# Optimization experiments

Measured on AMD Instinct MI355X. Metric: run time of the kernel, lower is better.

## Reference

```python
import jax, jax.numpy as jnp
import numpy as np
from jax import lax

B, H, W, DIM = 64, 32, 32, 448
HEADS, DH, WS = 8, 28, 8
INNER = DH * HEADS            # 224
C2 = DIM // 2                 # 224 (spatial branch channels == inner_dim)
HALF = INNER // 2             # 112 per attention sub-branch
SEQ_L1 = WS * WS              # 64 tokens per window
SEQ_L2 = (256 // HEADS) ** 2 // SEQ_L1  # 16 == number of windows (32x32 map)
SCALE = DH ** -0.5


def setup_inputs() -> dict:
    key = jax.random.key(0)
    ks = jax.random.split(key, 18)
    def nrm(k, shape, s):
        return jax.random.normal(k, shape, jnp.float32) * s
    inp = {}
    inp["x"] = jax.random.normal(ks[0], (B, H, W, DIM), jnp.float32)
    # trunc_normal_(std=1) positional biases -> clipped normals
    inp["pos_emb1"] = jnp.clip(jax.random.normal(ks[1], (1, 1, HEADS // 2, SEQ_L1, SEQ_L1), jnp.float32), -2.0, 2.0)
    inp["pos_emb2"] = jnp.clip(jax.random.normal(ks[2], (1, 1, HEADS // 2, SEQ_L2, SEQ_L2), jnp.float32), -2.0, 2.0)
    # linear weights stored (in, out)
    inp["Wq"] = nrm(ks[3], (C2, INNER), 0.02)
    inp["Wkv"] = nrm(ks[4], (C2, 2 * INNER), 0.02)
    inp["Wout"] = nrm(ks[5], (INNER, DIM), 0.02)
    inp["bout"] = nrm(ks[6], (DIM,), 0.02)
    # 3D conv weights (O, I, D, Kh, Kw), fan-in = 224*27 -> std ~ 0.01
    for i, name in enumerate(["convr", "conv1", "conv2", "conv3"]):
        inp[name + "_w"] = nrm(ks[7 + 2 * i], (C2, C2, 3, 3, 3), 0.01)
        inp[name + "_b"] = nrm(ks[8 + 2 * i], (C2,), 0.01)
    return inp


def _conv3d(t, w, b):
    y = lax.conv_general_dilated(t, w, (1, 1, 1), [(1, 1)] * 3,
                                 dimension_numbers=("NCDHW", "OIDHW", "NCDHW"))
    return y + b[None, :, None, None, None]


def _window(t):
    # [b, H, W, c] -> [b, n_windows, ws*ws, c]
    b, h, w, c = t.shape
    t = t.reshape(b, h // WS, WS, w // WS, WS, c).transpose(0, 1, 3, 2, 4, 5)
    return t.reshape(b, (h // WS) * (w // WS), WS * WS, c)


def _unwindow(t):
    # [b, n_windows, ws*ws, c] -> [b, H, W, c]
    b, n, m, c = t.shape
    t = t.reshape(b, H // WS, W // WS, WS, WS, c).transpose(0, 1, 3, 2, 4, 5)
    return t.reshape(b, H, W, c)


def _split_heads(t):
    # [b, n, m, half] -> [b, n, heads//2, m, dh]
    b, n, m, c = t.shape
    return t.reshape(b, n, m, HEADS // 2, DH).transpose(0, 1, 3, 2, 4)


def _merge_heads(t):
    # [b, n, heads//2, m, dh] -> [b, n, m, half]
    b, n, h, m, d = t.shape
    return t.transpose(0, 1, 3, 2, 4).reshape(b, n, m, h * d)


def _attn(q, q_, k, v, pos):
    del q_
    sim = jnp.einsum("bnhid,bnhjd->bnhij", q * SCALE, k) + pos
    a = jax.nn.softmax(sim, axis=-1)
    return jnp.einsum("bnhij,bnhjd->bnhid", a, v)


def reference(x, pos_emb1, pos_emb2, Wq, Wkv, Wout, bout,
              convr_w, convr_b, conv1_w, conv1_b, conv2_w, conv2_b, conv3_w, conv3_b):
    b = x.shape[0]
    x1 = x[..., :C2]
    x2 = x[..., C2:]
    # spectral 3D conv branch: [b, c2, 1, H, W]
    x2 = x2.transpose(0, 3, 1, 2)[:, :, None]
    res = jax.nn.relu(_conv3d(x2, convr_w, convr_b))
    o = jax.nn.relu(_conv3d(x2, conv1_w, conv1_b))
    o = jax.nn.relu(_conv3d(o, conv2_w, conv2_b))
    o = jax.nn.relu(_conv3d(o, conv3_w, conv3_b))
    X2S = (o + res)[:, :, 0].transpose(0, 2, 3, 1)  # [b, H, W, c2]

    q = x1 @ Wq
    kv = x1 @ Wkv
    k, v = kv[..., :INNER], kv[..., INNER:]
    q1, q2 = q[..., :HALF], q[..., HALF:]
    k1, k2 = k[..., :HALF], k[..., HALF:]
    v1, v2 = v[..., :HALF], v[..., HALF:]

    # local (within-window) branch
    q1h, k1h, v1h = map(lambda t: _split_heads(_window(t)), (q1, k1, v1))
    sim1 = jnp.einsum("bnhid,bnhjd->bnhij", q1h * SCALE, k1h) + pos_emb1
    out1 = jnp.einsum("bnhij,bnhjd->bnhid", jax.nn.softmax(sim1, axis=-1), v1h)
    out1 = _merge_heads(out1)  # [b, n, m, half]

    # grid (across-window) branch: swap window/token axes
    q2h, k2h, v2h = map(lambda t: _split_heads(_window(t).transpose(0, 2, 1, 3)), (q2, k2, v2))
    sim2 = jnp.einsum("bnhid,bnhjd->bnhij", q2h * SCALE, k2h) + pos_emb2
    out2 = jnp.einsum("bnhij,bnhjd->bnhid", jax.nn.softmax(sim2, axis=-1), v2h)
    out2 = _merge_heads(out2).transpose(0, 2, 1, 3)  # [b, n, m, half]

    out = jnp.concatenate([out1, out2], axis=-1) @ Wout + bout  # [b, n, m, DIM]
    out = _unwindow(out)
    return jnp.concatenate([out, X2S], axis=-1)  # [b, H, W, DIM + C2]
```

## Files before the change

### kernel.cpp

```cpp
#include <hip/hip_runtime.h>

typedef unsigned short u16;
typedef unsigned int   u32;
typedef __attribute__((ext_vector_type(4))) float  f32x4;
typedef __attribute__((ext_vector_type(8))) short  s16x8;
typedef __attribute__((ext_vector_type(8))) __bf16 bf16x8;
typedef __attribute__((ext_vector_type(2))) u32    u32x2;

#define DEV __device__ __forceinline__
#define SCALE_Q 0.1889822365046136f

DEV float bf2f(u16 u){ u32 x = ((u32)u)<<16; float f; __builtin_memcpy(&f,&x,4); return f; }
DEV u16   f2bf(float f){ u32 x; __builtin_memcpy(&x,&f,4); return (u16)((x + 0x7fffu + ((x>>16)&1u))>>16); }

DEV s16x8 cvt8(const float* __restrict__ src){
  f32x4 f0 = *(const f32x4*)src, f1 = *(const f32x4*)(src+4);
  bf16x8 b;
  b[0]=(__bf16)f0[0]; b[1]=(__bf16)f0[1]; b[2]=(__bf16)f0[2]; b[3]=(__bf16)f0[3];
  b[4]=(__bf16)f1[0]; b[5]=(__bf16)f1[1]; b[6]=(__bf16)f1[2]; b[7]=(__bf16)f1[3];
  return __builtin_bit_cast(s16x8, b);
}

DEV void ld28(const u16* __restrict__ p, float* dst, float scale){
#pragma unroll
  for (int j=0;j<7;j++){
    u32x2 w = *(const u32x2*)(p + j*4);
    dst[j*4+0] = bf2f((u16)(w[0]&0xffffu))*scale;
    dst[j*4+1] = bf2f((u16)(w[0]>>16))*scale;
    dst[j*4+2] = bf2f((u16)(w[1]&0xffffu))*scale;
    dst[j*4+3] = bf2f((u16)(w[1]>>16))*scale;
  }
}

__global__ void pack_k(const float* __restrict__ Wq, const float* __restrict__ Wkv,
                       const float* __restrict__ Wout,
                       const float* __restrict__ wr, const float* __restrict__ w1,
                       const float* __restrict__ w2, const float* __restrict__ w3,
                       u16* __restrict__ WqkvT, u16* __restrict__ WoutT,
                       u16* __restrict__ convW)
{
  int idx = blockIdx.x*256 + threadIdx.x;
  if (idx < 150528) {
    int nn = idx/224, k = idx - nn*224;
    float v;
    if (nn < 224)      v = Wq [k*224 + nn];
    else if (nn < 448) v = Wkv[k*448 + (nn-224)];
    else               v = Wkv[k*448 + (nn-448) + 224];
    WqkvT[idx] = f2bf(v);
  } else if (idx < 250880) {
    int j = idx - 150528;
    int nn = j/224, k = j - nn*224;
    WoutT[j] = f2bf(Wout[k*448 + nn]);
  } else {
    int j = idx - 250880;
    int cv = j/451584, rem = j - cv*451584;
    int co = rem/2016, kk = rem - co*2016;
    int tap = kk/224, ci = kk - tap*224;
    const float* w = (cv==0)?wr:(cv==1)?w1:(cv==2)?w2:w3;
    convW[j] = f2bf(w[(co*224 + ci)*27 + 9 + tap]);
  }
}

enum { M_QKV=0, M_CX2=1, M_CBF=2, M_C3=3, M_OUT=4 };

template<int MODE>
__global__ __launch_bounds__(512,2) void gemm_k(
    const void* __restrict__ Av, const u16* __restrict__ Bt,
    const float* __restrict__ bias, const u16* __restrict__ resid,
    void* __restrict__ Dv)
{
  constexpr bool CONV = (MODE==M_CX2 || MODE==M_CBF || MODE==M_C3);
  constexpr bool AF32 = (MODE==M_QKV || MODE==M_CX2);
  constexpr int KTOT = CONV ? 2016 : 224;
  constexpr int KS   = KTOT/32;
  constexpr int ASTR = AF32 ? 448 : 224;
  constexpr int AOFF = (MODE==M_CX2) ? 224 : 0;

  __shared__ __align__(16) u16 Als[128][40];
  __shared__ __align__(16) u16 Bls[224][40];

  const int t  = threadIdx.x;
  const int bm = blockIdx.x, nb = blockIdx.y;
  const int lane = t&63, lr = lane&15, lg = lane>>4;
  const int w = t>>6, wm = w>>1, wn = w&1;
  const int ar = t>>2, aq = t&3;
  const int p  = bm*128 + ar;
  const int pb = p>>10, py = (p>>5)&31, px = p&31;

  f32x4 acc[2][7];
  { f32x4 zf = {0.f,0.f,0.f,0.f};
#pragma unroll
    for (int i=0;i<2;i++)
#pragma unroll
      for (int j=0;j<7;j++) acc[i][j] = zf; }

  const s16x8 zv = {0,0,0,0,0,0,0,0};

  for (int ks=0; ks<KS; ++ks) {
    s16x8 av;
    if constexpr (CONV) {
      const int tap = ks/7, kc = ks - tap*7;
      const int dy = tap/3 - 1, dx = tap - (tap/3)*3 - 1;
      const int yy = py+dy, xx = px+dx;
      const bool ok = (yy>=0) & (yy<32) & (xx>=0) & (xx<32);
      const int yyc = yy<0?0:(yy>31?31:yy);
      const int xxc = xx<0?0:(xx>31?31:xx);
      const int off = ((pb*32+yyc)*32+xxc)*ASTR + AOFF + kc*32 + aq*8;
      s16x8 val;
      if constexpr (AF32) val = cvt8((const float*)Av + off);
      else                val = *(const s16x8*)((const u16*)Av + off);
      av = ok ? val : zv;
    } else {
      const int off = p*ASTR + ks*32 + aq*8;
      if constexpr (AF32) av = cvt8((const float*)Av + off);
      else                av = *(const s16x8*)((const u16*)Av + off);
    }
    const s16x8 bv0 = *(const s16x8*)(Bt + (nb*224 + (t>>2))*KTOT + ks*32 + aq*8);
    s16x8 bv1 = zv;
    if (t < 384)
      bv1 = *(const s16x8*)(Bt + (nb*224 + 128 + (t>>2))*KTOT + ks*32 + aq*8);

    __syncthreads();
    *(s16x8*)&Als[ar][aq*8] = av;
    *(s16x8*)&Bls[t>>2][aq*8] = bv0;
    if (t < 384) *(s16x8*)&Bls[128 + (t>>2)][aq*8] = bv1;
    __syncthreads();

    const bf16x8 af0 = *(const bf16x8*)&Als[wm*32 +      lr][lg*8];
    const bf16x8 af1 = *(const bf16x8*)&Als[wm*32 + 16 + lr][lg*8];
#pragma unroll
    for (int ni=0; ni<7; ++ni) {
      const bf16x8 bfr = *(const bf16x8*)&Bls[wn*112 + ni*16 + lr][lg*8];
      acc[0][ni] = __builtin_amdgcn_mfma_f32_16x16x32_bf16(af0, bfr, acc[0][ni], 0,0,0);
      acc[1][ni] = __builtin_amdgcn_mfma_f32_16x16x32_bf16(af1, bfr, acc[1][ni], 0,0,0);
    }
  }

#pragma unroll
  for (int mi=0; mi<2; ++mi) {
    const int rbase = bm*128 + wm*32 + mi*16 + lg*4;
#pragma unroll
    for (int ni=0; ni<7; ++ni) {
      const int col = wn*112 + ni*16 + lr;
      const int n   = nb*224 + col;
      float badd = 0.f;
      if constexpr (MODE != M_QKV) badd = bias[n];
#pragma unroll
      for (int r=0;r<4;r++){
        const int prow = rbase + r;
        float v = acc[mi][ni][r] + badd;
        if constexpr (CONV) v = fmaxf(v, 0.f);
        if constexpr (MODE==M_C3) {
          v += bf2f(resid[prow*224 + col]);
          ((float*)Dv)[prow*672 + 448 + col] = v;
        } else if constexpr (MODE==M_OUT) {
          ((float*)Dv)[prow*672 + n] = v;
        } else if constexpr (MODE==M_QKV) {
          ((u16*)Dv)[prow*672 + n] = f2bf(v);
        } else {
          ((u16*)Dv)[prow*224 + col] = f2bf(v);
        }
      }
    }
  }
}

__global__ __launch_bounds__(256,2) void attn1_k(const u16* __restrict__ qkv,
    const float* __restrict__ pos1, u16* __restrict__ attnout)
{
  __shared__ __align__(16) float KL[64][112];
  __shared__ __align__(16) float VL[64][112];
  const int t = threadIdx.x;
  const int b = blockIdx.x>>4, n = blockIdx.x&15;
  const int base = b*1024 + (n>>2)*256 + (n&3)*8;
  {
    const int r = t>>2, part = t&3;
    const int pr_ = base + (r>>3)*32 + (r&7);
    const u16* kp = qkv + pr_*672 + 224 + part*28;
    const u16* vp = kp + 224;
#pragma unroll
    for (int j=0;j<7;j++){
      u32x2 kk = *(const u32x2*)(kp + j*4);
      u32x2 vv = *(const u32x2*)(vp + j*4);
      const int c = part*28 + j*4;
      KL[r][c+0]=bf2f((u16)(kk[0]&0xffffu)); KL[r][c+1]=bf2f((u16)(kk[0]>>16));
      KL[r][c+2]=bf2f((u16)(kk[1]&0xffffu)); KL[r][c+3]=bf2f((u16)(kk[1]>>16));
      VL[r][c+0]=bf2f((u16)(vv[0]&0xffffu)); VL[r][c+1]=bf2f((u16)(vv[0]>>16));
      VL[r][c+2]=bf2f((u16)(vv[1]&0xffffu)); VL[r][c+3]=bf2f((u16)(vv[1]>>16));
    }
  }
  __syncthreads();

  const int h = t>>6, i = t&63;
  const int pi = base + (i>>3)*32 + (i&7);
  float q[28];
  ld28(qkv + pi*672 + h*28, q, SCALE_Q);

  float s[64];
  const float* pr = pos1 + (h*64+i)*64;
#pragma unroll
  for (int j4=0;j4<16;j4++){
    f32x4 pv = *(const f32x4*)(pr + j4*4);
    s[j4*4+0]=pv[0]; s[j4*4+1]=pv[1]; s[j4*4+2]=pv[2]; s[j4*4+3]=pv[3];
  }
  const int c0 = h*28;
#pragma unroll
  for (int j=0;j<64;j++){
    const f32x4* kr = (const f32x4*)&KL[j][c0];
    float a0=0.f,a1=0.f,a2=0.f,a3=0.f;
#pragma unroll
    for (int u=0;u<7;u++){
      f32x4 kv = kr[u];
      a0 += q[u*4+0]*kv[0]; a1 += q[u*4+1]*kv[1];
      a2 += q[u*4+2]*kv[2]; a3 += q[u*4+3]*kv[3];
    }
    s[j] += (a0+a1)+(a2+a3);
  }
  float mx = s[0];
#pragma unroll
  for (int j=1;j<64;j++) mx = fmaxf(mx, s[j]);
  float sum = 0.f;
#pragma unroll
  for (int j=0;j<64;j++){ float e = __expf(s[j]-mx); s[j]=e; sum+=e; }
  const float inv = 1.f/sum;

  float out[28];
#pragma unroll
  for (int u=0;u<28;u++) out[u]=0.f;
#pragma unroll
  for (int j=0;j<64;j++){
    const float pj = s[j];
    const f32x4* vr = (const f32x4*)&VL[j][c0];
#pragma unroll
    for (int u=0;u<7;u++){
      f32x4 vv = vr[u];
      out[u*4+0] += pj*vv[0]; out[u*4+1] += pj*vv[1];
      out[u*4+2] += pj*vv[2]; out[u*4+3] += pj*vv[3];
    }
  }
  u16* op = attnout + pi*224 + h*28;
#pragma unroll
  for (int u=0;u<7;u++){
    u32x2 wv;
    wv[0] = (u32)f2bf(out[u*4+0]*inv) | ((u32)f2bf(out[u*4+1]*inv)<<16);
    wv[1] = (u32)f2bf(out[u*4+2]*inv) | ((u32)f2bf(out[u*4+3]*inv)<<16);
    *(u32x2*)(op + u*4) = wv;
  }
}

__global__ __launch_bounds__(256,1) void attn2_k(const u16* __restrict__ qkv,
    const float* __restrict__ pos2, u16* __restrict__ attnout)
{
  const int t = threadIdx.x;
  const int b = blockIdx.x>>4, mg = blockIdx.x&15;
  const int m = mg*4 + (t>>6);
  const int lane = t&63, h = lane>>4, i = lane&15;
  const int base = b*1024 + (m>>3)*32 + (m&7);
  const int pi = base + (i>>2)*256 + (i&3)*8;

  float q[28];
  ld28(qkv + pi*672 + 112 + h*28, q, SCALE_Q);

  float s[16];
  const float* pr = pos2 + (h*16+i)*16;
#pragma unroll
  for (int j4=0;j4<4;j4++){
    f32x4 pv = *(const f32x4*)(pr + j4*4);
    s[j4*4+0]=pv[0]; s[j4*4+1]=pv[1]; s[j4*4+2]=pv[2]; s[j4*4+3]=pv[3];
  }
#pragma unroll
  for (int j=0;j<16;j++){
    const int pj_ = base + (j>>2)*256 + (j&3)*8;
    float kk[28];
    ld28(qkv + pj_*672 + 336 + h*28, kk, 1.0f);
    float a=0.f;
#pragma unroll
    for (int u=0;u<28;u++) a += q[u]*kk[u];
    s[j] += a;
  }
  float mx = s[0];
#pragma unroll
  for (int j=1;j<16;j++) mx = fmaxf(mx, s[j]);
  float sum = 0.f;
#pragma unroll
  for (int j=0;j<16;j++){ float e = __expf(s[j]-mx); s[j]=e; sum+=e; }
  const float inv = 1.f/sum;

  float out[28];
#pragma unroll
  for (int u=0;u<28;u++) out[u]=0.f;
#pragma unroll
  for (int j=0;j<16;j++){
    const int pj_ = base + (j>>2)*256 + (j&3)*8;
    float vv[28];
    ld28(qkv + pj_*672 + 560 + h*28, vv, 1.0f);
    const float pj = s[j];
#pragma unroll
    for (int u=0;u<28;u++) out[u] += pj*vv[u];
  }
  u16* op = attnout + pi*224 + 112 + h*28;
#pragma unroll
  for (int u=0;u<7;u++){
    u32x2 wv;
    wv[0] = (u32)f2bf(out[u*4+0]*inv) | ((u32)f2bf(out[u*4+1]*inv)<<16);
    wv[1] = (u32)f2bf(out[u*4+2]*inv) | ((u32)f2bf(out[u*4+3]*inv)<<16);
    *(u32x2*)(op + u*4) = wv;
  }
}

extern "C" void kernel_launch(void* const* d_in, const int* in_sizes, int n_in,
                              void* d_out, int out_size, void* d_ws, size_t ws_size,
                              hipStream_t stream) {
  const float* x    = (const float*)d_in[0];
  const float* pos1 = (const float*)d_in[1];
  const float* pos2 = (const float*)d_in[2];
  const float* Wq   = (const float*)d_in[3];
  const float* Wkv  = (const float*)d_in[4];
  const float* Wout = (const float*)d_in[5];
  const float* bout = (const float*)d_in[6];
  const float* wr   = (const float*)d_in[7];
  const float* br   = (const float*)d_in[8];
  const float* w1   = (const float*)d_in[9];
  const float* b1   = (const float*)d_in[10];
  const float* w2   = (const float*)d_in[11];
  const float* b2   = (const float*)d_in[12];
  const float* w3   = (const float*)d_in[13];
  const float* b3   = (const float*)d_in[14];

  char* ws = (char*)d_ws;
  const size_t SLOT = 65536ull*224*2;
  u16* res  = (u16*)(ws);
  u16* oA   = (u16*)(ws + SLOT);
  u16* oB   = (u16*)(ws + 2*SLOT);
  u16* qkv  = (u16*)(ws);
  u16* attnout = (u16*)(ws + 3*SLOT);
  u16* WqkvT   = (u16*)(ws + 4*SLOT);
  u16* WoutT   = WqkvT + 672*224;
  u16* convW   = WoutT + 448*224;
  float* dout  = (float*)d_out;

  pack_k<<<8036, 256, 0, stream>>>(Wq, Wkv, Wout, wr, w1, w2, w3, WqkvT, WoutT, convW);

  gemm_k<M_CX2><<<dim3(512,1), 512, 0, stream>>>(x,  convW + 0*451584, br, nullptr, res);
  gemm_k<M_CX2><<<dim3(512,1), 512, 0, stream>>>(x,  convW + 1*451584, b1, nullptr, oA);
  gemm_k<M_CBF><<<dim3(512,1), 512, 0, stream>>>(oA, convW + 2*451584, b2, nullptr, oB);
  gemm_k<M_C3 ><<<dim3(512,1), 512, 0, stream>>>(oB, convW + 3*451584, b3, res, dout);

  gemm_k<M_QKV><<<dim3(512,3), 512, 0, stream>>>(x, WqkvT, nullptr, nullptr, qkv);
  attn1_k<<<1024, 256, 0, stream>>>(qkv, pos1, attnout);
  attn2_k<<<1024, 256, 0, stream>>>(qkv, pos2, attnout);
  gemm_k<M_OUT><<<dim3(512,2), 512, 0, stream>>>(attnout, WoutT, bout, nullptr, dout);
}
```

Measured before the change: 555.1 us.

## Pad conv inputs, fuse first two convs, double-buffer GEMM with direct-to-LDS loads

```diff
diff --git a/kernel.cpp b/kernel.cpp
--- a/kernel.cpp
+++ b/kernel.cpp
@@ -19,6 +19,13 @@
   b[0]=(__bf16)f0[0]; b[1]=(__bf16)f0[1]; b[2]=(__bf16)f0[2]; b[3]=(__bf16)f0[3];
   b[4]=(__bf16)f1[0]; b[5]=(__bf16)f1[1]; b[6]=(__bf16)f1[2]; b[7]=(__bf16)f1[3];
   return __builtin_bit_cast(s16x8, b);
+}
+
+DEV void gll16(const u16* g, u16* l){
+  __builtin_amdgcn_global_load_lds(
+      (const __attribute__((address_space(1))) u32*)(const void*)g,
+      (__attribute__((address_space(3))) u32*)(void*)l,
+      16, 0, 0);
 }
 
 DEV void ld28(const u16* __restrict__ p, float* dst, float scale){
@@ -61,104 +68,143 @@
   }
 }
 
-enum { M_QKV=0, M_CX2=1, M_CBF=2, M_C3=3, M_OUT=4 };
+__global__ void prep_k(const float* __restrict__ x, u16* __restrict__ x1bf,
+                       u16* __restrict__ xpad, u16* __restrict__ oApad,
+                       u16* __restrict__ oBpad)
+{
+  int idx = blockIdx.x*256 + threadIdx.x;
+  int pp = idx/28, c8 = idx - pp*28;
+  int b = pp/1156, rem = pp - b*1156, y = rem/34, xx = rem - y*34;
+  int c0 = c8*8;
+  if (y>=1 && y<=32 && xx>=1 && xx<=32){
+    int p = (b*32 + y-1)*32 + (xx-1);
+    *(s16x8*)(x1bf + p*224 + c0) = cvt8(x + p*448 + c0);
+    *(s16x8*)(xpad + pp*224 + c0) = cvt8(x + p*448 + 224 + c0);
+  } else {
+    const s16x8 z = {0,0,0,0,0,0,0,0};
+    *(s16x8*)(xpad  + pp*224 + c0) = z;
+    *(s16x8*)(oApad + pp*224 + c0) = z;
+    *(s16x8*)(oBpad + pp*224 + c0) = z;
+  }
+}
+
+enum { M_FUSED=0, M_C2=1, M_C3=2, M_QKV=3, M_OUT=4 };
 
 template<int MODE>
-__global__ __launch_bounds__(512,2) void gemm_k(
-    const void* __restrict__ Av, const u16* __restrict__ Bt,
-    const float* __restrict__ bias, const u16* __restrict__ resid,
-    void* __restrict__ Dv)
+__global__ __launch_bounds__(512,1) void gemm_k(
+    const u16* __restrict__ A, const u16* __restrict__ Bt,
+    const float* __restrict__ bias0, const float* __restrict__ bias1,
+    u16* __restrict__ outA, u16* __restrict__ outB, float* __restrict__ outF)
 {
-  constexpr bool CONV = (MODE==M_CX2 || MODE==M_CBF || MODE==M_C3);
-  constexpr bool AF32 = (MODE==M_QKV || MODE==M_CX2);
+  constexpr bool CONV = (MODE==M_FUSED || MODE==M_C2 || MODE==M_C3);
   constexpr int KTOT = CONV ? 2016 : 224;
   constexpr int KS   = KTOT/32;
-  constexpr int ASTR = AF32 ? 448 : 224;
-  constexpr int AOFF = (MODE==M_CX2) ? 224 : 0;
-
-  __shared__ __align__(16) u16 Als[128][40];
-  __shared__ __align__(16) u16 Bls[224][40];
+
+  __shared__ __align__(16) u16 Als[2][256*32];
+  __shared__ __align__(16) u16 Bls[2][224*32];
 
   const int t  = threadIdx.x;
   const int bm = blockIdx.x, nb = blockIdx.y;
   const int lane = t&63, lr = lane&15, lg = lane>>4;
   const int w = t>>6, wm = w>>1, wn = w&1;
-  const int ar = t>>2, aq = t&3;
-  const int p  = bm*128 + ar;
-  const int pb = p>>10, py = (p>>5)&31, px = p&31;
-
-  f32x4 acc[2][7];
+  const int aq8 = (t&3)*8;
+
+  const int r0 = t>>2;
+  const int p0 = bm*256 + r0, p1 = p0 + 128;
+  int PP0=0, PP1=0;
+  if constexpr (CONV){
+    PP0 = ((p0>>10)*34 + ((p0>>5)&31) + 1)*34 + (p0&31) + 1;
+    PP1 = ((p1>>10)*34 + ((p1>>5)&31) + 1)*34 + (p1&31) + 1;
+  }
+  const int Bb0 = (nb*224 +       r0)*KTOT + aq8;
+  const int Bb1 = (nb*224 + 128 + r0)*KTOT + aq8;
+
+  u16* aL[2] = { &Als[0][0] + w*512, &Als[1][0] + w*512 };
+  u16* bL[2] = { &Bls[0][0] + w*512, &Bls[1][0] + w*512 };
+
+  auto STAGE = [&](int buf, int ks){
+    if constexpr (CONV){
+      const int tap = ks/7, kc = ks - tap*7;
+      const int ty = tap/3, tx = tap - ty*3;
+      const int toff = (ty-1)*34 + (tx-1);
+      const int ke = kc*32 + aq8;
+      gll16(A + (PP0+toff)*224 + ke, aL[buf]);
+      gll16(A + (PP1+toff)*224 + ke, aL[buf] + 4096);
+    } else {
+      gll16(A + p0*224 + ks*32 + aq8, aL[buf]);
+      gll16(A + p1*224 + ks*32 + aq8, aL[buf] + 4096);
+    }
+    gll16(Bt + Bb0 + ks*32, bL[buf]);
+    if (w < 6) gll16(Bt + Bb1 + ks*32, bL[buf] + 4096);
+  };
+
+  f32x4 acc[4][7];
   { f32x4 zf = {0.f,0.f,0.f,0.f};
 #pragma unroll
-    for (int i=0;i<2;i++)
+    for (int i=0;i<4;i++)
 #pragma unroll
       for (int j=0;j<7;j++) acc[i][j] = zf; }
 
-  const s16x8 zv = {0,0,0,0,0,0,0,0};
-
-  for (int ks=0; ks<KS; ++ks) {
-    s16x8 av;
-    if constexpr (CONV) {
-      const int tap = ks/7, kc = ks - tap*7;
-      const int dy = tap/3 - 1, dx = tap - (tap/3)*3 - 1;
-      const int yy = py+dy, xx = px+dx;
-      const bool ok = (yy>=0) & (yy<32) & (xx>=0) & (xx<32);
-      const int yyc = yy<0?0:(yy>31?31:yy);
-      const int xxc = xx<0?0:(xx>31?31:xx);
-      const int off = ((pb*32+yyc)*32+xxc)*ASTR + AOFF + kc*32 + aq*8;
-      s16x8 val;
-      if constexpr (AF32) val = cvt8((const float*)Av + off);
-      else                val = *(const s16x8*)((const u16*)Av + off);
-      av = ok ? val : zv;
-    } else {
-      const int off = p*ASTR + ks*32 + aq*8;
-      if constexpr (AF32) av = cvt8((const float*)Av + off);
-      else                av = *(const s16x8*)((const u16*)Av + off);
-    }
-    const s16x8 bv0 = *(const s16x8*)(Bt + (nb*224 + (t>>2))*KTOT + ks*32 + aq*8);
-    s16x8 bv1 = zv;
-    if (t < 384)
-      bv1 = *(const s16x8*)(Bt + (nb*224 + 128 + (t>>2))*KTOT + ks*32 + aq*8);
+  STAGE(0, 0);
+  __syncthreads();
+
+  for (int ks=0; ks<KS; ++ks){
+    const int cur = ks&1;
+    if (ks+1 < KS) STAGE(cur^1, ks+1);
+
+    const u16* Ac = &Als[cur][0];
+    const u16* Bc = &Bls[cur][0];
+    bf16x8 af[4], bfv[7];
+#pragma unroll
+    for (int mi=0; mi<4; ++mi)
+      af[mi] = *(const bf16x8*)(Ac + (wm*64 + mi*16 + lr)*32 + lg*8);
+#pragma unroll
+    for (int ni=0; ni<7; ++ni)
+      bfv[ni] = *(const bf16x8*)(Bc + (wn*112 + ni*16 + lr)*32 + lg*8);
+
+#pragma unroll
+    for (int ni=0; ni<7; ++ni)
+#pragma unroll
+      for (int mi=0; mi<4; ++mi)
+        acc[mi][ni] = __builtin_amdgcn_mfma_f32_16x16x32_bf16(af[mi], bfv[ni], acc[mi][ni], 0,0,0);
 
     __syncthreads();
-    *(s16x8*)&Als[ar][aq*8] = av;
-    *(s16x8*)&Bls[t>>2][aq*8] = bv0;
-    if (t < 384) *(s16x8*)&Bls[128 + (t>>2)][aq*8] = bv1;
-    __syncthreads();
-
-    const bf16x8 af0 = *(const bf16x8*)&Als[wm*32 +      lr][lg*8];
-    const bf16x8 af1 = *(const bf16x8*)&Als[wm*32 + 16 + lr][lg*8];
-#pragma unroll
-    for (int ni=0; ni<7; ++ni) {
-      const bf16x8 bfr = *(const bf16x8*)&Bls[wn*112 + ni*16 + lr][lg*8];
-      acc[0][ni] = __builtin_amdgcn_mfma_f32_16x16x32_bf16(af0, bfr, acc[0][ni], 0,0,0);
-      acc[1][ni] = __builtin_amdgcn_mfma_f32_16x16x32_bf16(af1, bfr, acc[1][ni], 0,0,0);
-    }
-  }
-
-#pragma unroll
-  for (int mi=0; mi<2; ++mi) {
-    const int rbase = bm*128 + wm*32 + mi*16 + lg*4;
-#pragma unroll
-    for (int ni=0; ni<7; ++ni) {
+  }
+
+  const float* bs;
+  if constexpr (MODE==M_FUSED) bs = (nb==0) ? bias0 : bias1;
+  else bs = bias0;
+
+#pragma unroll
+  for (int mi=0; mi<4; ++mi){
+    const int rbase = bm*256 + wm*64 + mi*16 + lg*4;
+#pragma unroll
+    for (int ni=0; ni<7; ++ni){
       const int col = wn*112 + ni*16 + lr;
-      const int n   = nb*224 + col;
-      float badd = 0.f;
-      if constexpr (MODE != M_QKV) badd = bias[n];
 #pragma unroll
       for (int r=0;r<4;r++){
-        const int prow = rbase + r;
-        float v = acc[mi][ni][r] + badd;
-        if constexpr (CONV) v = fmaxf(v, 0.f);
-        if constexpr (MODE==M_C3) {
-          v += bf2f(resid[prow*224 + col]);
-          ((float*)Dv)[prow*672 + 448 + col] = v;
-        } else if constexpr (MODE==M_OUT) {
-          ((float*)Dv)[prow*672 + n] = v;
-        } else if constexpr (MODE==M_QKV) {
-          ((u16*)Dv)[prow*672 + n] = f2bf(v);
+        const int row = rbase + r;
+        float v = acc[mi][ni][r];
+        if constexpr (MODE==M_FUSED){
+          v = fmaxf(v + bs[col], 0.f);
+          if (nb==0){
+            outF[row*672 + 448 + col] = v;
+          } else {
+            const int pp = ((row>>10)*34 + ((row>>5)&31) + 1)*34 + (row&31) + 1;
+            outB[pp*224 + col] = f2bf(v);
+          }
+        } else if constexpr (MODE==M_C2){
+          v = fmaxf(v + bs[col], 0.f);
+          const int pp = ((row>>10)*34 + ((row>>5)&31) + 1)*34 + (row&31) + 1;
+          outB[pp*224 + col] = f2bf(v);
+        } else if constexpr (MODE==M_C3){
+          v = fmaxf(v + bs[col], 0.f);
+          const int o = row*672 + 448 + col;
+          outF[o] = v + outF[o];
+        } else if constexpr (MODE==M_QKV){
+          outA[row*672 + nb*224 + col] = f2bf(v);
         } else {
-          ((u16*)Dv)[prow*224 + col] = f2bf(v);
+          outF[row*672 + nb*224 + col] = v + bs[nb*224 + col];
         }
       }
     }
@@ -328,26 +374,28 @@
   const float* b3   = (const float*)d_in[14];
 
   char* ws = (char*)d_ws;
-  const size_t SLOT = 65536ull*224*2;
-  u16* res  = (u16*)(ws);
-  u16* oA   = (u16*)(ws + SLOT);
-  u16* oB   = (u16*)(ws + 2*SLOT);
-  u16* qkv  = (u16*)(ws);
-  u16* attnout = (u16*)(ws + 3*SLOT);
-  u16* WqkvT   = (u16*)(ws + 4*SLOT);
-  u16* WoutT   = WqkvT + 672*224;
-  u16* convW   = WoutT + 448*224;
+  const size_t PADSZ = 73984ull*224*2;
+  const size_t FLATS = 65536ull*224*2;
+  u16* xpad   = (u16*)(ws);
+  u16* oApad  = (u16*)(ws + PADSZ);
+  u16* oBpad  = (u16*)(ws + 2*PADSZ);
+  u16* x1bf   = (u16*)(ws + 3*PADSZ);
+  u16* convW  = (u16*)(ws + 3*PADSZ + FLATS);
+  u16* WqkvT  = convW + 4*451584;
+  u16* WoutT  = WqkvT + 672*224;
+  u16* qkv     = (u16*)(ws);
+  u16* attnout = (u16*)(ws + 88080384);
   float* dout  = (float*)d_out;
 
   pack_k<<<8036, 256, 0, stream>>>(Wq, Wkv, Wout, wr, w1, w2, w3, WqkvT, WoutT, convW);
-
-  gemm_k<M_CX2><<<dim3(512,1), 512, 0, stream>>>(x,  convW + 0*451584, br, nullptr, res);
-  gemm_k<M_CX2><<<dim3(512,1), 512, 0, stream>>>(x,  convW + 1*451584, b1, nullptr, oA);
-  gemm_k<M_CBF><<<dim3(512,1), 512, 0, stream>>>(oA, convW + 2*451584, b2, nullptr, oB);
-  gemm_k<M_C3 ><<<dim3(512,1), 512, 0, stream>>>(oB, convW + 3*451584, b3, res, dout);
-
-  gemm_k<M_QKV><<<dim3(512,3), 512, 0, stream>>>(x, WqkvT, nullptr, nullptr, qkv);
+  prep_k<<<8092, 256, 0, stream>>>(x, x1bf, xpad, oApad, oBpad);
+
+  gemm_k<M_FUSED><<<dim3(256,2), 512, 0, stream>>>(xpad,  convW,          br, b1, nullptr, oApad, dout);
+  gemm_k<M_C2  ><<<dim3(256,1), 512, 0, stream>>>(oApad, convW+2*451584, b2, nullptr, nullptr, oBpad, nullptr);
+  gemm_k<M_C3  ><<<dim3(256,1), 512, 0, stream>>>(oBpad, convW+3*451584, b3, nullptr, nullptr, nullptr, dout);
+
+  gemm_k<M_QKV ><<<dim3(256,3), 512, 0, stream>>>(x1bf, WqkvT, nullptr, nullptr, qkv, nullptr, nullptr);
   attn1_k<<<1024, 256, 0, stream>>>(qkv, pos1, attnout);
   attn2_k<<<1024, 256, 0, stream>>>(qkv, pos2, attnout);
-  gemm_k<M_OUT><<<dim3(512,2), 512, 0, stream>>>(attnout, WoutT, bout, nullptr, dout);
-}
+  gemm_k<M_OUT ><<<dim3(256,2), 512, 0, stream>>>(attnout, WoutT, bout, nullptr, nullptr, nullptr, dout);
+}
```

New measurement: 613.2 us. +10.5%, slower.
